# Optimization experiments

Measured on AMD Instinct MI355X. Metric: run time of the kernel, lower is better.

Reference implementation:

```python
import jax, jax.numpy as jnp
import numpy as np

POOL = 7  # pool_size


def setup_inputs() -> dict:
    key = jax.random.key(0)
    k1, k2, k3, k4, k5 = jax.random.split(key, 5)
    img = jax.random.normal(k1, (1, 256, 256, 512), dtype=jnp.float32)
    # ROIs (x, y, w, h) as integers, guaranteed in-bounds: x+w<=256, y+h<=256
    x = jax.random.randint(k2, (1, 300), 0, 128)
    y = jax.random.randint(k3, (1, 300), 0, 128)
    w = jax.random.randint(k4, (1, 300), 16, 128)
    h = jax.random.randint(k5, (1, 300), 16, 128)
    rois = jnp.stack([x, y, w, h], axis=-1).astype(jnp.int32)  # (1, 300, 4)
    return {"img": img, "rois": rois}


def _axis_coords(start, size, full, pool):
    # tf.image.resize bilinear (v2, antialias=False): half-pixel centers,
    # src = (i + 0.5) * (in/out) - 0.5; floor/floor+1 clamped to [0, in-1].
    f = (jnp.arange(pool, dtype=jnp.float32) + 0.5) * size.astype(jnp.float32) / pool - 0.5
    f0 = jnp.floor(f)
    t = f - f0                                   # lerp weight in [0,1)
    i0 = jnp.clip(f0.astype(jnp.int32), 0, size - 1) + start
    i1 = jnp.clip(f0.astype(jnp.int32) + 1, 0, size - 1) + start
    return jnp.clip(i0, 0, full - 1), jnp.clip(i1, 0, full - 1), t


def _roi_bilinear(fmap, roi, pool):
    # fmap: (H, W, C); roi: (4,) int32 (x, y, w, h)
    H, W, _ = fmap.shape
    x, y, w, h = roi[0], roi[1], roi[2], roi[3]
    y0, y1, ty = _axis_coords(y, h, H, pool)
    x0, x1, tx = _axis_coords(x, w, W, pool)
    # Gather the 4 corner pixels directly: (P, P, C) each.
    tl = fmap[y0[:, None], x0[None, :]]
    tr = fmap[y0[:, None], x1[None, :]]
    bl = fmap[y1[:, None], x0[None, :]]
    br = fmap[y1[:, None], x1[None, :]]
    tx_ = tx[None, :, None]
    ty_ = ty[:, None, None]
    top = tl + (tr - tl) * tx_
    bot = bl + (br - bl) * tx_
    return top + (bot - top) * ty_


def reference(img, rois):
    # img: (1, H, W, C); rois: (1, num_rois, 4) int (x, y, w, h)
    pooled = jax.vmap(lambda r: _roi_bilinear(img[0], r, POOL))(rois[0])
    return pooled[None]  # (1, num_rois, POOL, POOL, C)
```

## Files before the change

### kernel.cpp

```cpp
#include <hip/hip_runtime.h>

#define POOL  7
#define CH    512
#define IMG_H 256
#define IMG_W 256

__global__ void __launch_bounds__(128)
roi_align_kernel(const float* __restrict__ img,
                 const int* __restrict__ rois,
                 float* __restrict__ out)
{
    const int bid = blockIdx.x;
    const int px  = bid % POOL;
    const int py  = (bid / POOL) % POOL;
    const int r   = bid / (POOL * POOL);

    const int x = rois[r * 4 + 0];
    const int y = rois[r * 4 + 1];
    const int w = rois[r * 4 + 2];
    const int h = rois[r * 4 + 3];

    const float fx  = (px + 0.5f) * (float)w / (float)POOL - 0.5f;
    const float fx0 = floorf(fx);
    const float tx  = fx - fx0;
    const int   ifx = (int)fx0;
    const int   x0  = min(max(min(max(ifx,     0), w - 1) + x, 0), IMG_W - 1);
    const int   x1  = min(max(min(max(ifx + 1, 0), w - 1) + x, 0), IMG_W - 1);

    const float fy  = (py + 0.5f) * (float)h / (float)POOL - 0.5f;
    const float fy0 = floorf(fy);
    const float ty  = fy - fy0;
    const int   ify = (int)fy0;
    const int   y0  = min(max(min(max(ify,     0), h - 1) + y, 0), IMG_H - 1);
    const int   y1  = min(max(min(max(ify + 1, 0), h - 1) + y, 0), IMG_H - 1);

    const float4* tl = (const float4*)(img + ((size_t)y0 * IMG_W + x0) * CH);
    const float4* tr = (const float4*)(img + ((size_t)y0 * IMG_W + x1) * CH);
    const float4* bl = (const float4*)(img + ((size_t)y1 * IMG_W + x0) * CH);
    const float4* br = (const float4*)(img + ((size_t)y1 * IMG_W + x1) * CH);

    const int c4 = threadIdx.x;

    const float4 a = tl[c4];
    const float4 b = tr[c4];
    const float4 c = bl[c4];
    const float4 d = br[c4];

    float4 res;
    {
        float tpx = a.x + (b.x - a.x) * tx;
        float tpy = a.y + (b.y - a.y) * tx;
        float tpz = a.z + (b.z - a.z) * tx;
        float tpw = a.w + (b.w - a.w) * tx;
        float btx = c.x + (d.x - c.x) * tx;
        float bty = c.y + (d.y - c.y) * tx;
        float btz = c.z + (d.z - c.z) * tx;
        float btw = c.w + (d.w - c.w) * tx;
        res.x = tpx + (btx - tpx) * ty;
        res.y = tpy + (bty - tpy) * ty;
        res.z = tpz + (btz - tpz) * ty;
        res.w = tpw + (btw - tpw) * ty;
    }

    float4* o = (float4*)(out + (size_t)bid * CH);
    o[c4] = res;
}

extern "C" void kernel_launch(void* const* d_in, const int* in_sizes, int n_in,
                              void* d_out, int out_size, void* d_ws, size_t ws_size,
                              hipStream_t stream)
{
    const float* img  = (const float*)d_in[0];
    const int*   rois = (const int*)d_in[1];
    float*       out  = (float*)d_out;

    const int n_rois  = in_sizes[1] / 4;
    const int nblocks = n_rois * POOL * POOL;

    roi_align_kernel<<<nblocks, 128, 0, stream>>>(img, rois, out);
}
```

Measured before the change: 26.69 us.

## Process a full pooled row per block with batched loads and nontemporal stores

Each block now handles one pooled row (7 output bins) of an ROI instead of a single bin. Two 128-thread halves split the bins and each thread issues up to 16 vector loads before doing any interpolation. Outputs are written with nontemporal stores. The aim is more memory-level parallelism per thread, less per-block launch and ROI-decode overhead, and less cache pollution from the output. In exchange there are 7x fewer blocks, the halves are imbalanced (4 bins versus 3), and register pressure rises.

Result: no change. 26.40 us (-1.1%).

```diff
diff --git a/kernel.cpp b/kernel.cpp
--- a/kernel.cpp
+++ b/kernel.cpp
@@ -5,27 +5,21 @@
 #define IMG_H 256
 #define IMG_W 256
 
-__global__ void __launch_bounds__(128)
+typedef float f32x4 __attribute__((ext_vector_type(4)));
+
+__global__ void __launch_bounds__(256)
 roi_align_kernel(const float* __restrict__ img,
                  const int* __restrict__ rois,
                  float* __restrict__ out)
 {
     const int bid = blockIdx.x;
-    const int px  = bid % POOL;
-    const int py  = (bid / POOL) % POOL;
-    const int r   = bid / (POOL * POOL);
+    const int py  = bid % POOL;
+    const int r   = bid / POOL;
 
     const int x = rois[r * 4 + 0];
     const int y = rois[r * 4 + 1];
     const int w = rois[r * 4 + 2];
     const int h = rois[r * 4 + 3];
-
-    const float fx  = (px + 0.5f) * (float)w / (float)POOL - 0.5f;
-    const float fx0 = floorf(fx);
-    const float tx  = fx - fx0;
-    const int   ifx = (int)fx0;
-    const int   x0  = min(max(min(max(ifx,     0), w - 1) + x, 0), IMG_W - 1);
-    const int   x1  = min(max(min(max(ifx + 1, 0), w - 1) + x, 0), IMG_W - 1);
 
     const float fy  = (py + 0.5f) * (float)h / (float)POOL - 0.5f;
     const float fy0 = floorf(fy);
@@ -34,36 +28,46 @@
     const int   y0  = min(max(min(max(ify,     0), h - 1) + y, 0), IMG_H - 1);
     const int   y1  = min(max(min(max(ify + 1, 0), h - 1) + y, 0), IMG_H - 1);
 
-    const float4* tl = (const float4*)(img + ((size_t)y0 * IMG_W + x0) * CH);
-    const float4* tr = (const float4*)(img + ((size_t)y0 * IMG_W + x1) * CH);
-    const float4* bl = (const float4*)(img + ((size_t)y1 * IMG_W + x0) * CH);
-    const float4* br = (const float4*)(img + ((size_t)y1 * IMG_W + x1) * CH);
+    const int c4   = threadIdx.x & 127;
+    const int half = threadIdx.x >> 7;
 
-    const int c4 = threadIdx.x;
+    const float* row0 = img + (size_t)y0 * IMG_W * CH;
+    const float* row1 = img + (size_t)y1 * IMG_W * CH;
 
-    const float4 a = tl[c4];
-    const float4 b = tr[c4];
-    const float4 c = bl[c4];
-    const float4 d = br[c4];
+    f32x4 A[4], B[4], C[4], D[4];
+    float txs[4];
 
-    float4 res;
-    {
-        float tpx = a.x + (b.x - a.x) * tx;
-        float tpy = a.y + (b.y - a.y) * tx;
-        float tpz = a.z + (b.z - a.z) * tx;
-        float tpw = a.w + (b.w - a.w) * tx;
-        float btx = c.x + (d.x - c.x) * tx;
-        float bty = c.y + (d.y - c.y) * tx;
-        float btz = c.z + (d.z - c.z) * tx;
-        float btw = c.w + (d.w - c.w) * tx;
-        res.x = tpx + (btx - tpx) * ty;
-        res.y = tpy + (bty - tpy) * ty;
-        res.z = tpz + (btz - tpz) * ty;
-        res.w = tpw + (btw - tpw) * ty;
+    #pragma unroll
+    for (int k = 0; k < 4; ++k) {
+        const int px = half + 2 * k;
+        if (px < POOL) {
+            const float fx  = (px + 0.5f) * (float)w / (float)POOL - 0.5f;
+            const float fx0 = floorf(fx);
+            txs[k] = fx - fx0;
+            const int ifx = (int)fx0;
+            const int x0  = min(max(min(max(ifx,     0), w - 1) + x, 0), IMG_W - 1);
+            const int x1  = min(max(min(max(ifx + 1, 0), w - 1) + x, 0), IMG_W - 1);
+            A[k] = *(const f32x4*)(row0 + (size_t)x0 * CH + c4 * 4);
+            B[k] = *(const f32x4*)(row0 + (size_t)x1 * CH + c4 * 4);
+            C[k] = *(const f32x4*)(row1 + (size_t)x0 * CH + c4 * 4);
+            D[k] = *(const f32x4*)(row1 + (size_t)x1 * CH + c4 * 4);
+        }
     }
 
-    float4* o = (float4*)(out + (size_t)bid * CH);
-    o[c4] = res;
+    #pragma unroll
+    for (int k = 0; k < 4; ++k) {
+        const int px = half + 2 * k;
+        if (px < POOL) {
+            const float tx = txs[k];
+            const f32x4 a = A[k], b = B[k], c = C[k], d = D[k];
+            const f32x4 top = a + (b - a) * tx;
+            const f32x4 bot = c + (d - c) * tx;
+            const f32x4 res = top + (bot - top) * ty;
+
+            f32x4* o = (f32x4*)(out + ((size_t)(r * POOL * POOL + py * POOL + px)) * CH);
+            __builtin_nontemporal_store(res, o + c4);
+        }
+    }
 }
 
 extern "C" void kernel_launch(void* const* d_in, const int* in_sizes, int n_in,
@@ -75,7 +79,7 @@
     float*       out  = (float*)d_out;
 
     const int n_rois  = in_sizes[1] / 4;
-    const int nblocks = n_rois * POOL * POOL;
+    const int nblocks = n_rois * POOL;
 
-    roi_align_kernel<<<nblocks, 128, 0, stream>>>(img, rois, out);
+    roi_align_kernel<<<nblocks, 256, 0, stream>>>(img, rois, out);
 }
```
